# Performance work log

Measured on AMD Instinct MI355X. Metric: run time of the kernel, lower is better.

## Reference

```python
import jax, jax.numpy as jnp
import numpy as np

V, D, H, L, B, S = 32000, 512, 512, 2, 64, 64
PAD = 0
NEG = -1000000000.0


def setup_inputs() -> dict:
    key = jax.random.key(0)
    ks = jax.random.split(key, 12)
    s = 0.05
    X = jax.random.randint(ks[0], (B, S), 0, V)
    enc = jax.random.normal(ks[1], (B, S - 1, H), jnp.float32)
    mask = jnp.zeros((S - 1, S - 1), dtype=bool)
    emb = jax.random.normal(ks[2], (V, D), jnp.float32) * s
    lstm_Wih = jax.random.normal(ks[3], (L, 4 * H, D), jnp.float32) * s  # D == H so stacking works for layer>0
    lstm_Whh = jax.random.normal(ks[4], (L, 4 * H, H), jnp.float32) * s
    lstm_bih = jax.random.normal(ks[5], (L, 4 * H), jnp.float32) * s
    lstm_bhh = jax.random.normal(ks[6], (L, 4 * H), jnp.float32) * s
    attn_Wh = jax.random.normal(ks[7], (H, H), jnp.float32) * s  # attn weight cols acting on decoder hidden
    attn_We = jax.random.normal(ks[8], (H, H), jnp.float32) * s  # attn weight cols acting on encoder outputs
    attn_b = jax.random.normal(ks[9], (H,), jnp.float32) * s
    v_w = jax.random.normal(ks[10], (H,), jnp.float32) * s
    fc_W = jax.random.normal(ks[11], (V, 2 * H), jnp.float32) * s
    fc_b = jnp.zeros((V,), jnp.float32)
    return {"X": X, "encoderOutputs": enc, "mask": mask, "emb": emb,
            "lstm_Wih": lstm_Wih, "lstm_Whh": lstm_Whh, "lstm_bih": lstm_bih, "lstm_bhh": lstm_bhh,
            "attn_Wh": attn_Wh, "attn_We": attn_We, "attn_b": attn_b, "v_w": v_w,
            "fc_W": fc_W, "fc_b": fc_b}


def _forward(X, enc, mask, emb, Wih, Whh, bih, bhh, attn_Wh, attn_We, attn_b, v_w, fc_W, fc_b):
    Bn, Sn = X.shape
    T = Sn - 1
    E = emb[X[:, :-1]]  # [B,T,D]
    # encoder part of attention projection is time-invariant: hoist out of the loop
    enc_proj = jnp.einsum('beh,kh->bek', enc, attn_We) + attn_b  # [B,T,H]
    h0 = jnp.zeros((L, Bn, H), E.dtype)
    c0 = jnp.zeros((L, Bn, H), E.dtype)
    xs = (jnp.transpose(E, (1, 0, 2)), X[:, 1:].T, jnp.arange(T))

    def step(carry, x_t):
        h, c = carry
        e_t, tgt, t = x_t
        inp = e_t
        hs, cs = [], []
        for l in range(L):  # fixed small layer loop
            g = inp @ Wih[l].T + h[l] @ Whh[l].T + bih[l] + bhh[l]
            i, f, gg, o = jnp.split(g, 4, axis=-1)  # torch gate order i,f,g,o
            cn = jax.nn.sigmoid(f) * c[l] + jax.nn.sigmoid(i) * jnp.tanh(gg)
            hn = jax.nn.sigmoid(o) * jnp.tanh(cn)
            hs.append(hn); cs.append(cn)
            inp = hn
        h = jnp.stack(hs); c = jnp.stack(cs)
        top = inp  # [B,H] == LSTM output of last layer
        energy = jnp.tanh((top @ attn_Wh.T)[:, None, :] + enc_proj)  # [B,T,H]
        scores = energy @ v_w  # [B,T]
        # original: self.mask[t-1] (python negative wrap) then mask.unsqueeze(0).unsqueeze(1)
        m = mask[(t - 1) % mask.shape[0], :T]  # [T]
        s3 = jnp.where(m[None, None, :], NEG, scores[None])  # broadcast -> [1,B,T]
        att = jax.nn.softmax(s3, axis=1)[0]  # softmax over batch dim, as in original
        weighted = jnp.einsum('be,beh->bh', att, enc)
        logits = jnp.concatenate([top, weighted], axis=1) @ fc_W.T + fc_b  # [B,V]
        logp = jax.nn.log_softmax(logits, axis=-1)
        nll = -jnp.take_along_axis(logp, tgt[:, None], axis=1)[:, 0]
        valid = tgt != PAD
        loss_t = jnp.sum(jnp.where(valid, nll, 0.0)) / jnp.sum(valid)  # CE mean with ignore_index
        return (h, c), loss_t

    _, losses = jax.lax.scan(step, (h0, c0), xs)
    return jnp.mean(losses)  # totalLoss / (seq_len - 1)


def reference(X, encoderOutputs, mask, emb, lstm_Wih, lstm_Whh, lstm_bih, lstm_bhh, attn_Wh, attn_We, attn_b, v_w, fc_W, fc_b):
    return _forward(X, encoderOutputs, mask, emb, lstm_Wih, lstm_Whh, lstm_bih, lstm_bhh, attn_Wh, attn_We, attn_b, v_w, fc_W, fc_b)
```

## Files before the change

### kernel.cpp

```cpp
#include <hip/hip_runtime.h>
#include <math.h>

#define NEGV -1000000000.0f

typedef unsigned short u16;
typedef __attribute__((ext_vector_type(8))) short bf16x8;
typedef __attribute__((ext_vector_type(4))) float f32x4;

__device__ __forceinline__ u16 f2bf(float f){
  union { float f; unsigned u; } v; v.f = f;
  unsigned u = v.u;
  unsigned r = (u + 0x7fffu + ((u >> 16) & 1u)) >> 16;
  return (u16)r;
}
__device__ __forceinline__ float bf2f(u16 b){
  union { unsigned u; float f; } v; v.u = ((unsigned)b) << 16;
  return v.f;
}
__device__ __forceinline__ float sigmf(float x){ return 1.f / (1.f + __expf(-x)); }
__device__ __forceinline__ float tanhf_(float x){
  float e = __expf(-2.f * fabsf(x));
  float t = (1.f - e) / (1.f + e);
  return x >= 0.f ? t : -t;
}
__device__ __forceinline__ float wred64(float v){
  #pragma unroll
  for (int m = 32; m; m >>= 1) v += __shfl_xor(v, m, 64);
  return v;
}
__device__ __forceinline__ float wmax64(float v){
  #pragma unroll
  for (int m = 32; m; m >>= 1) v = fmaxf(v, __shfl_xor(v, m, 64));
  return v;
}

typedef const __attribute__((address_space(1))) unsigned int* gas_ptr;
typedef __attribute__((address_space(3))) unsigned int* las_ptr;
__device__ __forceinline__ void gl_lds16(const u16* g, u16* l){
  __builtin_amdgcn_global_load_lds((gas_ptr)g, (las_ptr)l, 16, 0, 0);
}

__device__ __forceinline__ void st_sc1_u16(u16* p, unsigned v){
  asm volatile("global_store_short %0, %1, off sc1" :: "v"(p), "v"(v) : "memory");
}

__global__ __launch_bounds__(256) void k_prep(
    const float* wih, const float* whh, const float* we, const float* wh,
    const float* fcw, const float* enc, const float* bih, const float* bhh,
    u16* wihb, u16* whhb, u16* web, u16* whb, u16* fcwb, u16* encb, float* b01)
{
  const long n0 = 2097152, n1 = 2097152, n2 = 262144, n3 = 262144;
  const long n4 = 32768000, n5 = 2064384, n6 = 4096;
  const long total = n0 + n1 + n2 + n3 + n4 + n5 + n6;
  long stride = (long)gridDim.x * 256;
  for (long i = (long)blockIdx.x * 256 + threadIdx.x; i < total; i += stride){
    long j = i;
    if (j < n0){ wihb[j] = f2bf(wih[j]); continue; } j -= n0;
    if (j < n1){ whhb[j] = f2bf(whh[j]); continue; } j -= n1;
    if (j < n2){ web[j]  = f2bf(we[j]);  continue; } j -= n2;
    if (j < n3){ whb[j]  = f2bf(wh[j]);  continue; } j -= n3;
    if (j < n4){ fcwb[j] = f2bf(fcw[j]); continue; } j -= n4;
    if (j < n5){ encb[j] = f2bf(enc[j]); continue; } j -= n5;
    b01[j] = bih[j] + bhh[j];
  }
}

__global__ __launch_bounds__(256) void k_embed(const int* X, const float* emb, u16* ebf){
  int row = blockIdx.x;
  int t = row >> 6, b = row & 63;
  int tok = X[b * 64 + t];
  const float* src = emb + (long)tok * 512;
  u16* dst = ebf + (long)row * 512;
  for (int j = threadIdx.x; j < 512; j += 256) dst[j] = f2bf(src[j]);
}

__global__ __launch_bounds__(256) void gemm_bt(
    const u16* Am, int lda, const u16* Bm, int ldb,
    float* C, int ldc, const float* bias, int K)
{
  __shared__ u16 sA[64 * 32], sB[64 * 32];
  int tm = blockIdx.x, tn = blockIdx.y;
  int tid = threadIdx.x;
  int wave = tid >> 6, lane = tid & 63;
  int wm = wave >> 1, wn = wave & 1;
  int q = lane >> 4, cl = lane & 15;
  f32x4 acc[2][2];
  #pragma unroll
  for (int i = 0; i < 2; i++)
    #pragma unroll
    for (int j = 0; j < 2; j++) acc[i][j] = (f32x4){0.f, 0.f, 0.f, 0.f};

  int r = tid >> 2, ck = tid & 3;
  const u16* Ags = Am + (long)(tm * 64 + r) * lda + ck * 8;
  const u16* Bgs = Bm + (long)(tn * 64 + r) * ldb + ck * 8;
  u16* sAw = &sA[wave * 512];
  u16* sBw = &sB[wave * 512];

  for (int kt = 0; kt < K; kt += 32){
    gl_lds16(Ags + kt, sAw);
    gl_lds16(Bgs + kt, sBw);
    __syncthreads();
    #pragma unroll
    for (int i = 0; i < 2; i++){
      bf16x8 af = *(const bf16x8*)&sA[(wm * 32 + i * 16 + cl) * 32 + q * 8];
      #pragma unroll
      for (int j = 0; j < 2; j++){
        bf16x8 bfv = *(const bf16x8*)&sB[(wn * 32 + j * 16 + cl) * 32 + q * 8];
        acc[i][j] = __builtin_amdgcn_mfma_f32_16x16x32_bf16(af, bfv, acc[i][j], 0, 0, 0);
      }
    }
    __syncthreads();
  }
  #pragma unroll
  for (int i = 0; i < 2; i++)
    #pragma unroll
    for (int j = 0; j < 2; j++){
      int colg = tn * 64 + wn * 32 + j * 16 + cl;
      float bv = bias ? bias[colg] : 0.f;
      #pragma unroll
      for (int rr = 0; rr < 4; rr++){
        int rowg = tm * 64 + wm * 32 + i * 16 + q * 4 + rr;
        C[(long)rowg * ldc + colg] = acc[i][j][rr] + bv;
      }
    }
}

__global__ __launch_bounds__(256) void gemm_btb(
    const u16* Am, int lda, const u16* Bm, int ldb,
    u16* C, int ldc, const float* bias, int K)
{
  __shared__ u16 sA[64 * 32], sB[64 * 32];
  int tm = blockIdx.x, tn = blockIdx.y;
  int tid = threadIdx.x;
  int wave = tid >> 6, lane = tid & 63;
  int wm = wave >> 1, wn = wave & 1;
  int q = lane >> 4, cl = lane & 15;
  f32x4 acc[2][2];
  #pragma unroll
  for (int i = 0; i < 2; i++)
    #pragma unroll
    for (int j = 0; j < 2; j++) acc[i][j] = (f32x4){0.f, 0.f, 0.f, 0.f};

  int r = tid >> 2, ck = tid & 3;
  const u16* Ags = Am + (long)(tm * 64 + r) * lda + ck * 8;
  const u16* Bgs = Bm + (long)(tn * 64 + r) * ldb + ck * 8;
  u16* sAw = &sA[wave * 512];
  u16* sBw = &sB[wave * 512];

  for (int kt = 0; kt < K; kt += 32){
    gl_lds16(Ags + kt, sAw);
    gl_lds16(Bgs + kt, sBw);
    __syncthreads();
    #pragma unroll
    for (int i = 0; i < 2; i++){
      bf16x8 af = *(const bf16x8*)&sA[(wm * 32 + i * 16 + cl) * 32 + q * 8];
      #pragma unroll
      for (int j = 0; j < 2; j++){
        bf16x8 bfv = *(const bf16x8*)&sB[(wn * 32 + j * 16 + cl) * 32 + q * 8];
        acc[i][j] = __builtin_amdgcn_mfma_f32_16x16x32_bf16(af, bfv, acc[i][j], 0, 0, 0);
      }
    }
    __syncthreads();
  }
  #pragma unroll
  for (int i = 0; i < 2; i++)
    #pragma unroll
    for (int j = 0; j < 2; j++){
      int colg = tn * 64 + wn * 32 + j * 16 + cl;
      float bv = bias ? bias[colg] : 0.f;
      #pragma unroll
      for (int rr = 0; rr < 4; rr++){
        int rowg = tm * 64 + wm * 32 + i * 16 + q * 4 + rr;
        C[(long)rowg * ldc + colg] = f2bf(acc[i][j][rr] + bv);
      }
    }
}

__device__ __forceinline__ void wait_flags(int* flags, int tid, int need0, int need1){
  if (tid < 64){
    int need = (tid < 32) ? need0 : need1;
    for (;;){
      int v = __hip_atomic_load(flags + tid, __ATOMIC_RELAXED, __HIP_MEMORY_SCOPE_AGENT);
      if (__ballot(v >= need) == ~0ull) break;
    }
  }
  __syncthreads();
}

#define ISSUE_RING_FRAGS(afr, Ab)                                              \
  {                                                                            \
    _Pragma("unroll")                                                          \
    for (int kt = 0; kt < 16; kt++)                                            \
      asm volatile("global_load_dwordx4 %0, %1, off offset:%2 sc1"             \
                   : "=v"(afr[kt]) : "v"(Ab), "i"(kt * 64));                   \
  }
#define WAITCNT_VM(N)                                                          \
  { asm volatile("s_waitcnt vmcnt(" #N ")" ::: "memory");                      \
    __builtin_amdgcn_sched_barrier(0); }

__global__ __launch_bounds__(256, 1) void lstm_pipe(
    const u16* whh0, const u16* wih1, const u16* whh1,
    const u16* x0b, const float* b1s,
    u16* ring0, u16* ring1, u16* feat, int* flags)
{
  __shared__ u16 sW[32768];
  __shared__ u16 sW2[32768];
  int wg = blockIdx.x;
  int layer = wg >> 5;
  int cc = (wg & 31) * 16;
  int tid = threadIdx.x;
  int wave = tid >> 6, lane = tid & 63;
  int q = lane >> 4, cl = lane & 15;
  int j = cc + cl;

  {
    const u16* src = layer ? whh1 : whh0;
    for (int ch = tid; ch < 4096; ch += 256){
      int row = ch >> 6, c = ch & 63;
      int g = row >> 4, r = row & 15;
      *(uint4*)&sW[((c * 4 + g) * 16 + r) * 8] =
          *(const uint4*)&src[(long)(g * 512 + cc + r) * 512 + c * 8];
      if (layer)
        *(uint4*)&sW2[((c * 4 + g) * 16 + r) * 8] =
            *(const uint4*)&wih1[(long)(g * 512 + cc + r) * 512 + c * 8];
    }
  }
  __syncthreads();

  float cst[4] = {0.f, 0.f, 0.f, 0.f};
  float bg[4];
  if (layer){
    #pragma unroll
    for (int g = 0; g < 4; g++) bg[g] = b1s[g * 512 + j];
  }

  int foff = (wave * 16 + cl) * 512 + q * 8;

  for (int t = 0; t < 63; t++){
    f32x4 acc[4];
    #pragma unroll
    for (int g = 0; g < 4; g++) acc[g] = (f32x4){0.f, 0.f, 0.f, 0.f};

    if (layer == 0){
      float xg[4][4];
      #pragma unroll
      for (int rr = 0; rr < 4; rr++){
        int s = wave * 16 + q * 4 + rr;
        const u16* xr = x0b + (long)(t * 64 + s) * 2048 + j;
        #pragma unroll
        for (int g = 0; g < 4; g++) xg[g][rr] = bf2f(xr[g * 512]);
      }
      wait_flags(flags, tid, t, t - 7);
      {
        const u16* Ab = ring0 + ((t + 7) & 7) * 32768 + foff;
        bf16x8 afr[16];
        ISSUE_RING_FRAGS(afr, Ab);
        WAITCNT_VM(0);
        #pragma unroll
        for (int kt = 0; kt < 16; kt++)
          #pragma unroll
          for (int g = 0; g < 4; g++){
            bf16x8 bfv = *(const bf16x8*)&sW[(((kt * 4 + q) * 4 + g) * 16 + cl) * 8];
            acc[g] = __builtin_amdgcn_mfma_f32_16x16x32_bf16(afr[kt], bfv, acc[g], 0, 0, 0);
          }
      }
      u16* hn = ring0 + (t & 7) * 32768;
      #pragma unroll
      for (int rr = 0; rr < 4; rr++){
        int s = wave * 16 + q * 4 + rr;
        float gi = acc[0][rr] + xg[0][rr];
        float gf = acc[1][rr] + xg[1][rr];
        float gg = acc[2][rr] + xg[2][rr];
        float go = acc[3][rr] + xg[3][rr];
        float cn = sigmf(gf) * cst[rr] + sigmf(gi) * tanhf_(gg);
        cst[rr] = cn;
        st_sc1_u16(hn + s * 512 + j, (unsigned)f2bf(sigmf(go) * tanhf_(cn)));
      }
    } else {
      wait_flags(flags, tid, t + 1, t);
      const u16* Ab1 = ring1 + ((t + 7) & 7) * 32768 + foff;
      const u16* Ab0 = ring0 + (t & 7) * 32768 + foff;
      bf16x8 a1[16], a0[16];
      ISSUE_RING_FRAGS(a1, Ab1);
      ISSUE_RING_FRAGS(a0, Ab0);
      WAITCNT_VM(16);
      #pragma unroll
      for (int kt = 0; kt < 16; kt++)
        #pragma unroll
        for (int g = 0; g < 4; g++){
          bf16x8 bfv = *(const bf16x8*)&sW[(((kt * 4 + q) * 4 + g) * 16 + cl) * 8];
          acc[g] = __builtin_amdgcn_mfma_f32_16x16x32_bf16(a1[kt], bfv, acc[g], 0, 0, 0);
        }
      WAITCNT_VM(0);
      #pragma unroll
      for (int kt = 0; kt < 16; kt++)
        #pragma unroll
        for (int g = 0; g < 4; g++){
          bf16x8 bfv = *(const bf16x8*)&sW2[(((kt * 4 + q) * 4 + g) * 16 + cl) * 8];
          acc[g] = __builtin_amdgcn_mfma_f32_16x16x32_bf16(a0[kt], bfv, acc[g], 0, 0, 0);
        }
      u16* hn = ring1 + (t & 7) * 32768;
      #pragma unroll
      for (int rr = 0; rr < 4; rr++){
        int s = wave * 16 + q * 4 + rr;
        float gi = acc[0][rr] + bg[0];
        float gf = acc[1][rr] + bg[1];
        float gg = acc[2][rr] + bg[2];
        float go = acc[3][rr] + bg[3];
        float cn = sigmf(gf) * cst[rr] + sigmf(gi) * tanhf_(gg);
        cst[rr] = cn;
        u16 hb = f2bf(sigmf(go) * tanhf_(cn));
        st_sc1_u16(hn + s * 512 + j, (unsigned)hb);
        feat[(long)(t * 64 + s) * 1024 + j] = hb;
      }
    }
    asm volatile("s_waitcnt vmcnt(0)" ::: "memory");
    __syncthreads();
    if (tid == 0)
      __hip_atomic_store(flags + wg, t + 1, __ATOMIC_RELAXED, __HIP_MEMORY_SCOPE_AGENT);
  }
}

__global__ __launch_bounds__(256) void k_scores(
    const float* qb, const float* encp, const float* vw, float* scores)
{
  int row = blockIdx.x;
  int b = row & 63;
  int wave = threadIdx.x >> 6, lane = threadIdx.x & 63;
  float qv[8], vwv[8];
  const float* qr = qb + (long)row * 512 + lane * 8;
  #pragma unroll
  for (int i = 0; i < 8; i++){ qv[i] = qr[i]; vwv[i] = vw[lane * 8 + i]; }
  for (int e = wave; e < 63; e += 4){
    const float* er = encp + (long)(b * 63 + e) * 512 + lane * 8;
    float s = 0.f;
    #pragma unroll
    for (int i = 0; i < 8; i++) s += vwv[i] * tanhf_(qv[i] + er[i]);
    s = wred64(s);
    if (lane == 0) scores[(long)row * 63 + e] = s;
  }
}

__global__ __launch_bounds__(64) void k_att(float* scores, const unsigned char* mask){
  int idx = blockIdx.x;
  int t = idx / 63, e = idx - t * 63;
  int lane = threadIdx.x;
  long off = (long)(t * 64 + lane) * 63 + e;
  float s = scores[off];
  if (mask[((t + 62) % 63) * 63 + e]) s = NEGV;
  float M = wmax64(s);
  float p = __expf(s - M);
  float S = wred64(p);
  scores[off] = p / S;
}

__global__ __launch_bounds__(256) void k_weighted(
    const float* att, const float* enc, u16* feat)
{
  int row = blockIdx.x;
  int b = row & 63;
  int j = threadIdx.x;
  float a0 = 0.f, a1 = 0.f;
  const float* ar = att + (long)row * 63;
  const float* er = enc + (long)b * 63 * 512;
  for (int e = 0; e < 63; e++){
    float a = ar[e];
    a0 += a * er[(long)e * 512 + j];
    a1 += a * er[(long)e * 512 + j + 256];
  }
  feat[(long)row * 1024 + 512 + j] = f2bf(a0);
  feat[(long)row * 1024 + 768 + j] = f2bf(a1);
}

__global__ __launch_bounds__(256) void gemm_fc(
    const u16* Am, const u16* Bm, const float* fcb, float* partials)
{
  __shared__ u16 sA[128 * 32], sB[128 * 32];
  __shared__ float sm[128][2], ss[128][2];
  int tm = blockIdx.x, tn = blockIdx.y;
  int tid = threadIdx.x;
  int wave = tid >> 6, lane = tid & 63;
  int wm = wave >> 1, wn = wave & 1;
  int q = lane >> 4, cl = lane & 15;
  f32x4 acc[4][4];
  #pragma unroll
  for (int i = 0; i < 4; i++)
    #pragma unroll
    for (int j = 0; j < 4; j++) acc[i][j] = (f32x4){0.f, 0.f, 0.f, 0.f};

  const u16 *Ag[2], *Bg[2];
  u16 *sAd[2], *sBd[2];
  #pragma unroll
  for (int h = 0; h < 2; h++){
    int idx = h * 256 + tid, rr = idx >> 2, ck = idx & 3;
    Ag[h] = Am + (long)(tm * 128 + rr) * 1024 + ck * 8;
    Bg[h] = Bm + (long)(tn * 128 + rr) * 1024 + ck * 8;
    sAd[h] = &sA[(h * 4 + wave) * 512];
    sBd[h] = &sB[(h * 4 + wave) * 512];
  }
  for (int kt = 0; kt < 1024; kt += 32){
    #pragma unroll
    for (int h = 0; h < 2; h++){
      gl_lds16(Ag[h] + kt, sAd[h]);
      gl_lds16(Bg[h] + kt, sBd[h]);
    }
    __syncthreads();
    bf16x8 afr[4];
    #pragma unroll
    for (int mt = 0; mt < 4; mt++)
      afr[mt] = *(const bf16x8*)&sA[(wm * 64 + mt * 16 + cl) * 32 + q * 8];
    #pragma unroll
    for (int nt = 0; nt < 4; nt++){
      bf16x8 bfv = *(const bf16x8*)&sB[(wn * 64 + nt * 16 + cl) * 32 + q * 8];
      #pragma unroll
      for (int mt = 0; mt < 4; mt++)
        acc[mt][nt] = __builtin_amdgcn_mfma_f32_16x16x32_bf16(afr[mt], bfv, acc[mt][nt], 0, 0, 0);
    }
    __syncthreads();
  }
  float fb[4];
  #pragma unroll
  for (int nt = 0; nt < 4; nt++) fb[nt] = fcb[tn * 128 + wn * 64 + nt * 16 + cl];
  #pragma unroll
  for (int mt = 0; mt < 4; mt++){
    #pragma unroll
    for (int rr = 0; rr < 4; rr++){
      float vals[4];
      float vm = -3.0e38f, vs = 0.f;
      #pragma unroll
      for (int nt = 0; nt < 4; nt++){ float v = acc[mt][nt][rr] + fb[nt]; vals[nt] = v; vm = fmaxf(vm, v); }
      #pragma unroll
      for (int nt = 0; nt < 4; nt++) vs += __expf(vals[nt] - vm);
      #pragma unroll
      for (int m = 1; m < 16; m <<= 1){
        float om = __shfl_xor(vm, m, 16);
        float os = __shfl_xor(vs, m, 16);
        float nm = fmaxf(vm, om);
        vs = vs * __expf(vm - nm) + os * __expf(om - nm);
        vm = nm;
      }
      if (cl == 0){ int rl = wm * 64 + mt * 16 + q * 4 + rr; sm[rl][wn] = vm; ss[rl][wn] = vs; }
    }
  }
  __syncthreads();
  if (tid < 128){
    float m0 = sm[tid][0], m1 = sm[tid][1];
    float M = fmaxf(m0, m1);
    float S = ss[tid][0] * __expf(m0 - M) + ss[tid][1] * __expf(m1 - M);
    long row = tm * 128 + tid;
    partials[(row * 250 + tn) * 2]     = M;
    partials[(row * 250 + tn) * 2 + 1] = S;
  }
}

__global__ __launch_bounds__(256) void k_rowstats(
    const float* partials, const u16* feat, const u16* fcwb,
    const float* fcb, const int* X, float* nll)
{
  int row = blockIdx.x * 4 + (threadIdx.x >> 6);
  int lane = threadIdx.x & 63;
  if (row >= 4032) return;
  float vm = -3.0e38f, vs = 0.f;
  const float* pr = partials + (long)row * 500;
  for (int i = lane; i < 250; i += 64){
    float m = pr[i * 2], s2 = pr[i * 2 + 1];
    float nm = fmaxf(vm, m);
    vs = vs * __expf(vm - nm) + s2 * __expf(m - nm);
    vm = nm;
  }
  #pragma unroll
  for (int m = 32; m; m >>= 1){
    float om = __shfl_xor(vm, m, 64);
    float os = __shfl_xor(vs, m, 64);
    float nm = fmaxf(vm, om);
    vs = vs * __expf(vm - nm) + os * __expf(om - nm);
    vm = nm;
  }
  float logZ = vm + __logf(vs);
  int t = row >> 6, b = row & 63;
  int tgt = X[b * 64 + t + 1];
  const u16* fr = feat + (long)row * 1024 + lane * 16;
  const u16* wr = fcwb + (long)tgt * 1024 + lane * 16;
  float d = 0.f;
  #pragma unroll
  for (int i = 0; i < 16; i++) d += bf2f(fr[i]) * bf2f(wr[i]);
  d = wred64(d);
  if (lane == 0) nll[row] = logZ - (d + fcb[tgt]);
}

__global__ __launch_bounds__(256) void k_final(const float* nll, const int* X, float* out){
  __shared__ float lt[64];
  int wave = threadIdx.x >> 6, lane = threadIdx.x & 63;
  for (int t = wave; t < 63; t += 4){
    int tgt = X[lane * 64 + t + 1];
    float v = (tgt != 0) ? nll[t * 64 + lane] : 0.f;
    float c = (tgt != 0) ? 1.f : 0.f;
    v = wred64(v); c = wred64(c);
    if (lane == 0) lt[t] = v / c;
  }
  __syncthreads();
  if (threadIdx.x == 0){
    float s = 0.f;
    for (int t = 0; t < 63; t++) s += lt[t];
    out[0] = s / 63.f;
  }
}

extern "C" void kernel_launch(void* const* d_in, const int* in_sizes, int n_in,
                              void* d_out, int out_size, void* d_ws, size_t ws_size,
                              hipStream_t stream)
{
  (void)in_sizes; (void)n_in; (void)out_size; (void)ws_size;
  const int*   X    = (const int*)d_in[0];
  const float* enc  = (const float*)d_in[1];
  const unsigned char* mask = (const unsigned char*)d_in[2];
  const float* emb  = (const float*)d_in[3];
  const float* wih  = (const float*)d_in[4];
  const float* whh  = (const float*)d_in[5];
  const float* bih  = (const float*)d_in[6];
  const float* bhh  = (const float*)d_in[7];
  const float* awh  = (const float*)d_in[8];
  const float* awe  = (const float*)d_in[9];
  const float* ab   = (const float*)d_in[10];
  const float* vw   = (const float*)d_in[11];
  const float* fcw  = (const float*)d_in[12];
  const float* fcb  = (const float*)d_in[13];
  float* out = (float*)d_out;

  char* w = (char*)d_ws;
  size_t o = 0;
  auto alloc = [&](size_t bytes){ size_t r = o; o = (o + bytes + 255) & ~(size_t)255; return r; };
  size_t o_ebf  = alloc((size_t)4032 * 512 * 2);
  size_t o_wihb = alloc((size_t)2 * 2048 * 512 * 2);
  size_t o_whhb = alloc((size_t)2 * 2048 * 512 * 2);
  size_t o_web  = alloc((size_t)512 * 512 * 2);
  size_t o_whb  = alloc((size_t)512 * 512 * 2);
  size_t o_fcwb = alloc((size_t)32000 * 1024 * 2);
  size_t o_encb = alloc((size_t)4032 * 512 * 2);
  size_t o_b01  = alloc((size_t)4096 * 4);
  size_t o_x0   = alloc((size_t)4032 * 2048 * 2);
  size_t o_encp = alloc((size_t)4032 * 512 * 4);
  size_t o_q    = alloc((size_t)4032 * 512 * 4);
  size_t o_feat = alloc((size_t)4096 * 1024 * 2);
  size_t o_ring = alloc((size_t)2 * 8 * 32768 * 2);
  size_t o_flags= alloc((size_t)256);
  size_t o_sc   = alloc((size_t)63 * 64 * 63 * 4);
  size_t o_part = alloc((size_t)4096 * 250 * 2 * 4);
  size_t o_nll  = alloc((size_t)4032 * 4);

  u16* ebf   = (u16*)(w + o_ebf);
  u16* wihb  = (u16*)(w + o_wihb);
  u16* whhb  = (u16*)(w + o_whhb);
  u16* web   = (u16*)(w + o_web);
  u16* whb   = (u16*)(w + o_whb);
  u16* fcwb  = (u16*)(w + o_fcwb);
  u16* encb  = (u16*)(w + o_encb);
  float* b01 = (float*)(w + o_b01);
  u16* x0b   = (u16*)(w + o_x0);
  float* encp= (float*)(w + o_encp);
  float* qb  = (float*)(w + o_q);
  u16* feat  = (u16*)(w + o_feat);
  u16* ring0 = (u16*)(w + o_ring);
  u16* ring1 = ring0 + 8 * 32768;
  int* flags = (int*)(w + o_flags);
  float* sc  = (float*)(w + o_sc);
  float* part= (float*)(w + o_part);
  float* nllb= (float*)(w + o_nll);

  hipMemsetAsync(w + o_ring, 0, (o_flags - o_ring) + 256, stream);

  k_prep<<<4096, 256, 0, stream>>>(wih, whh, awe, awh, fcw, enc, bih, bhh,
                                   wihb, whhb, web, whb, fcwb, encb, b01);
  k_embed<<<4032, 256, 0, stream>>>(X, emb, ebf);

  gemm_btb<<<dim3(63, 32), 256, 0, stream>>>(ebf, 512, wihb, 512, x0b, 2048, b01, 512);
  gemm_bt<<<dim3(63, 8), 256, 0, stream>>>(encb, 512, web, 512, encp, 512, ab, 512);

  lstm_pipe<<<64, 256, 0, stream>>>(whhb, wihb + 2048 * 512, whhb + 2048 * 512,
                                    x0b, b01 + 2048, ring0, ring1, feat, flags);

  gemm_bt<<<dim3(63, 8), 256, 0, stream>>>(feat, 1024, whb, 512, qb, 512, nullptr, 512);
  k_scores<<<4032, 256, 0, stream>>>(qb, encp, vw, sc);
  k_att<<<3969, 64, 0, stream>>>(sc, mask);
  k_weighted<<<4032, 256, 0, stream>>>(sc, enc, feat);

  gemm_fc<<<dim3(32, 250), 256, 0, stream>>>(feat, fcwb, fcb, part);
  k_rowstats<<<1008, 256, 0, stream>>>(part, feat, fcwb, fcb, X, nllb);
  k_final<<<1, 256, 0, stream>>>(nllb, X, out);
}
```

Before: 1.298 ms.

## Merge LSTM layers into one wavefront-skewed pipeline on 32 blocks

The persistent LSTM kernel now runs both layers in each of 32 workgroups instead of giving each layer its own 32 workgroups. Layer 1 runs one step behind layer 0, so both share a single global barrier per step. Per-block flag polling is replaced by a per-step atomic counter with sleep-based spinning. Layer 1's input weights are now read from global memory (L2) instead of LDS, since LDS only holds the two recurrent matrices. This halves the number of participating blocks and the barrier traffic, at the cost of more serial MFMA work per block per step and extra global weight reads.

Result: slower. 1.819 ms (+40.1%).

```diff
diff --git a/kernel.cpp b/kernel.cpp
--- a/kernel.cpp
+++ b/kernel.cpp
@@ -176,16 +176,6 @@
     }
 }
 
-__device__ __forceinline__ void wait_flags(int* flags, int tid, int need0, int need1){
-  if (tid < 64){
-    int need = (tid < 32) ? need0 : need1;
-    for (;;){
-      int v = __hip_atomic_load(flags + tid, __ATOMIC_RELAXED, __HIP_MEMORY_SCOPE_AGENT);
-      if (__ballot(v >= need) == ~0ull) break;
-    }
-  }
-  __syncthreads();
-}
 
 #define ISSUE_RING_FRAGS(afr, Ab)                                              \
   {                                                                            \
@@ -201,48 +191,39 @@
 __global__ __launch_bounds__(256, 1) void lstm_pipe(
     const u16* whh0, const u16* wih1, const u16* whh1,
     const u16* x0b, const float* b1s,
-    u16* ring0, u16* ring1, u16* feat, int* flags)
-{
-  __shared__ u16 sW[32768];
-  __shared__ u16 sW2[32768];
+    u16* ring0, u16* ring1, u16* feat, int* done)
+{
+  __shared__ u16 sW0[32768];
+  __shared__ u16 sW1[32768];
   int wg = blockIdx.x;
-  int layer = wg >> 5;
-  int cc = (wg & 31) * 16;
+  int cc = wg * 16;
   int tid = threadIdx.x;
   int wave = tid >> 6, lane = tid & 63;
   int q = lane >> 4, cl = lane & 15;
   int j = cc + cl;
 
-  {
-    const u16* src = layer ? whh1 : whh0;
-    for (int ch = tid; ch < 4096; ch += 256){
-      int row = ch >> 6, c = ch & 63;
-      int g = row >> 4, r = row & 15;
-      *(uint4*)&sW[((c * 4 + g) * 16 + r) * 8] =
-          *(const uint4*)&src[(long)(g * 512 + cc + r) * 512 + c * 8];
-      if (layer)
-        *(uint4*)&sW2[((c * 4 + g) * 16 + r) * 8] =
-            *(const uint4*)&wih1[(long)(g * 512 + cc + r) * 512 + c * 8];
-    }
+  for (int ch = tid; ch < 4096; ch += 256){
+    int row = ch >> 6, c = ch & 63;
+    int g = row >> 4, r = row & 15;
+    *(uint4*)&sW0[((c * 4 + g) * 16 + r) * 8] =
+        *(const uint4*)&whh0[(long)(g * 512 + cc + r) * 512 + c * 8];
+    *(uint4*)&sW1[((c * 4 + g) * 16 + r) * 8] =
+        *(const uint4*)&whh1[(long)(g * 512 + cc + r) * 512 + c * 8];
   }
   __syncthreads();
 
-  float cst[4] = {0.f, 0.f, 0.f, 0.f};
+  float cst0[4] = {0.f, 0.f, 0.f, 0.f};
+  float cst1[4] = {0.f, 0.f, 0.f, 0.f};
   float bg[4];
-  if (layer){
-    #pragma unroll
-    for (int g = 0; g < 4; g++) bg[g] = b1s[g * 512 + j];
-  }
+  #pragma unroll
+  for (int g = 0; g < 4; g++) bg[g] = b1s[g * 512 + j];
 
   int foff = (wave * 16 + cl) * 512 + q * 8;
-
-  for (int t = 0; t < 63; t++){
-    f32x4 acc[4];
-    #pragma unroll
-    for (int g = 0; g < 4; g++) acc[g] = (f32x4){0.f, 0.f, 0.f, 0.f};
-
-    if (layer == 0){
-      float xg[4][4];
+  const u16* wbase = wih1 + (long)(cc + cl) * 512 + q * 8;
+
+  for (int t = 0; t < 64; t++){
+    float xg[4][4];
+    if (t < 63){
       #pragma unroll
       for (int rr = 0; rr < 4; rr++){
         int s = wave * 16 + q * 4 + rr;
@@ -250,74 +231,90 @@
         #pragma unroll
         for (int g = 0; g < 4; g++) xg[g][rr] = bf2f(xr[g * 512]);
       }
-      wait_flags(flags, tid, t, t - 7);
-      {
-        const u16* Ab = ring0 + ((t + 7) & 7) * 32768 + foff;
-        bf16x8 afr[16];
-        ISSUE_RING_FRAGS(afr, Ab);
-        WAITCNT_VM(0);
-        #pragma unroll
-        for (int kt = 0; kt < 16; kt++)
-          #pragma unroll
-          for (int g = 0; g < 4; g++){
-            bf16x8 bfv = *(const bf16x8*)&sW[(((kt * 4 + q) * 4 + g) * 16 + cl) * 8];
-            acc[g] = __builtin_amdgcn_mfma_f32_16x16x32_bf16(afr[kt], bfv, acc[g], 0, 0, 0);
-          }
-      }
-      u16* hn = ring0 + (t & 7) * 32768;
-      #pragma unroll
-      for (int rr = 0; rr < 4; rr++){
-        int s = wave * 16 + q * 4 + rr;
-        float gi = acc[0][rr] + xg[0][rr];
-        float gf = acc[1][rr] + xg[1][rr];
-        float gg = acc[2][rr] + xg[2][rr];
-        float go = acc[3][rr] + xg[3][rr];
-        float cn = sigmf(gf) * cst[rr] + sigmf(gi) * tanhf_(gg);
-        cst[rr] = cn;
-        st_sc1_u16(hn + s * 512 + j, (unsigned)f2bf(sigmf(go) * tanhf_(cn)));
-      }
-    } else {
-      wait_flags(flags, tid, t + 1, t);
-      const u16* Ab1 = ring1 + ((t + 7) & 7) * 32768 + foff;
-      const u16* Ab0 = ring0 + (t & 7) * 32768 + foff;
-      bf16x8 a1[16], a0[16];
-      ISSUE_RING_FRAGS(a1, Ab1);
-      ISSUE_RING_FRAGS(a0, Ab0);
-      WAITCNT_VM(16);
+    }
+    if (t > 0){
+      if (tid < 64){
+        const int* dp = done + (t - 1);
+        for (;;){
+          int v = __hip_atomic_load(dp, __ATOMIC_RELAXED, __HIP_MEMORY_SCOPE_AGENT);
+          if (__ballot(v >= 32)) break;
+          __builtin_amdgcn_s_sleep(1);
+        }
+      }
+      __syncthreads();
+    }
+
+    bf16x8 a0[16], a1[16];
+    const u16* Ab0 = ring0 + ((t + 7) & 7) * 32768 + foff;
+    const u16* Ab1 = ring1 + ((t + 6) & 7) * 32768 + foff;
+    ISSUE_RING_FRAGS(a0, Ab0);
+    ISSUE_RING_FRAGS(a1, Ab1);
+    WAITCNT_VM(16);
+
+    if (t < 63){
+      f32x4 acc0[4];
+      #pragma unroll
+      for (int g = 0; g < 4; g++) acc0[g] = (f32x4){0.f, 0.f, 0.f, 0.f};
       #pragma unroll
       for (int kt = 0; kt < 16; kt++)
         #pragma unroll
         for (int g = 0; g < 4; g++){
-          bf16x8 bfv = *(const bf16x8*)&sW[(((kt * 4 + q) * 4 + g) * 16 + cl) * 8];
-          acc[g] = __builtin_amdgcn_mfma_f32_16x16x32_bf16(a1[kt], bfv, acc[g], 0, 0, 0);
+          bf16x8 bfv = *(const bf16x8*)&sW0[(((kt * 4 + q) * 4 + g) * 16 + cl) * 8];
+          acc0[g] = __builtin_amdgcn_mfma_f32_16x16x32_bf16(a0[kt], bfv, acc0[g], 0, 0, 0);
         }
-      WAITCNT_VM(0);
+      u16* hn = ring0 + (t & 7) * 32768;
+      #pragma unroll
+      for (int rr = 0; rr < 4; rr++){
+        int s = wave * 16 + q * 4 + rr;
+        float gi = acc0[0][rr] + xg[0][rr];
+        float gf = acc0[1][rr] + xg[1][rr];
+        float gg = acc0[2][rr] + xg[2][rr];
+        float go = acc0[3][rr] + xg[3][rr];
+        float cn = sigmf(gf) * cst0[rr] + sigmf(gi) * tanhf_(gg);
+        cst0[rr] = cn;
+        st_sc1_u16(hn + s * 512 + j, (unsigned)f2bf(sigmf(go) * tanhf_(cn)));
+      }
+    }
+
+    if (t > 0){
+      f32x4 acc1[4];
+      #pragma unroll
+      for (int g = 0; g < 4; g++) acc1[g] = (f32x4){0.f, 0.f, 0.f, 0.f};
       #pragma unroll
       for (int kt = 0; kt < 16; kt++)
         #pragma unroll
         for (int g = 0; g < 4; g++){
-          bf16x8 bfv = *(const bf16x8*)&sW2[(((kt * 4 + q) * 4 + g) * 16 + cl) * 8];
-          acc[g] = __builtin_amdgcn_mfma_f32_16x16x32_bf16(a0[kt], bfv, acc[g], 0, 0, 0);
+          bf16x8 bfv = *(const bf16x8*)(wbase + (long)g * 262144 + kt * 32);
+          acc1[g] = __builtin_amdgcn_mfma_f32_16x16x32_bf16(a0[kt], bfv, acc1[g], 0, 0, 0);
         }
-      u16* hn = ring1 + (t & 7) * 32768;
+      WAITCNT_VM(0);
+      #pragma unroll
+      for (int kt = 0; kt < 16; kt++)
+        #pragma unroll
+        for (int g = 0; g < 4; g++){
+          bf16x8 bfv = *(const bf16x8*)&sW1[(((kt * 4 + q) * 4 + g) * 16 + cl) * 8];
+          acc1[g] = __builtin_amdgcn_mfma_f32_16x16x32_bf16(a1[kt], bfv, acc1[g], 0, 0, 0);
+        }
+      u16* hn = ring1 + ((t + 7) & 7) * 32768;
       #pragma unroll
       for (int rr = 0; rr < 4; rr++){
         int s = wave * 16 + q * 4 + rr;
-        float gi = acc[0][rr] + bg[0];
-        float gf = acc[1][rr] + bg[1];
-        float gg = acc[2][rr] + bg[2];
-        float go = acc[3][rr] + bg[3];
-        float cn = sigmf(gf) * cst[rr] + sigmf(gi) * tanhf_(gg);
-        cst[rr] = cn;
+        float gi = acc1[0][rr] + bg[0];
+        float gf = acc1[1][rr] + bg[1];
+        float gg = acc1[2][rr] + bg[2];
+        float go = acc1[3][rr] + bg[3];
+        float cn = sigmf(gf) * cst1[rr] + sigmf(gi) * tanhf_(gg);
+        cst1[rr] = cn;
         u16 hb = f2bf(sigmf(go) * tanhf_(cn));
         st_sc1_u16(hn + s * 512 + j, (unsigned)hb);
-        feat[(long)(t * 64 + s) * 1024 + j] = hb;
-      }
-    }
+        feat[(long)((t - 1) * 64 + s) * 1024 + j] = hb;
+      }
+    }
+
     asm volatile("s_waitcnt vmcnt(0)" ::: "memory");
     __syncthreads();
     if (tid == 0)
-      __hip_atomic_store(flags + wg, t + 1, __ATOMIC_RELAXED, __HIP_MEMORY_SCOPE_AGENT);
+      (void)__hip_atomic_fetch_add(done + t, 1, __ATOMIC_RELAXED, __HIP_MEMORY_SCOPE_AGENT);
   }
 }
 
@@ -543,7 +540,7 @@
   size_t o_q    = alloc((size_t)4032 * 512 * 4);
   size_t o_feat = alloc((size_t)4096 * 1024 * 2);
   size_t o_ring = alloc((size_t)2 * 8 * 32768 * 2);
-  size_t o_flags= alloc((size_t)256);
+  size_t o_done = alloc((size_t)256);
   size_t o_sc   = alloc((size_t)63 * 64 * 63 * 4);
   size_t o_part = alloc((size_t)4096 * 250 * 2 * 4);
   size_t o_nll  = alloc((size_t)4032 * 4);
@@ -562,12 +559,12 @@
   u16* feat  = (u16*)(w + o_feat);
   u16* ring0 = (u16*)(w + o_ring);
   u16* ring1 = ring0 + 8 * 32768;
-  int* flags = (int*)(w + o_flags);
+  int* done  = (int*)(w + o_done);
   float* sc  = (float*)(w + o_sc);
   float* part= (float*)(w + o_part);
   float* nllb= (float*)(w + o_nll);
 
-  hipMemsetAsync(w + o_ring, 0, (o_flags - o_ring) + 256, stream);
+  hipMemsetAsync(w + o_ring, 0, (o_done - o_ring) + 256, stream);
 
   k_prep<<<4096, 256, 0, stream>>>(wih, whh, awe, awh, fcw, enc, bih, bhh,
                                    wihb, whhb, web, whb, fcwb, encb, b01);
@@ -576,8 +573,8 @@
   gemm_btb<<<dim3(63, 32), 256, 0, stream>>>(ebf, 512, wihb, 512, x0b, 2048, b01, 512);
   gemm_bt<<<dim3(63, 8), 256, 0, stream>>>(encb, 512, web, 512, encp, 512, ab, 512);
 
-  lstm_pipe<<<64, 256, 0, stream>>>(whhb, wihb + 2048 * 512, whhb + 2048 * 512,
-                                    x0b, b01 + 2048, ring0, ring1, feat, flags);
+  lstm_pipe<<<32, 256, 0, stream>>>(whhb, wihb + 2048 * 512, whhb + 2048 * 512,
+                                    x0b, b01 + 2048, ring0, ring1, feat, done);
 
   gemm_bt<<<dim3(63, 8), 256, 0, stream>>>(feat, 1024, whb, 512, qb, 512, nullptr, 512);
   k_scores<<<4032, 256, 0, stream>>>(qb, encp, vw, sc);
```

## Use per-step counters for LSTM pipeline sync and double-buffer FC GEMM tiles

Applied to the files above, without the earlier changes.

Each LSTM pipeline step now waits on a single per-timestep atomic counter that the 32 workgroups of a layer increment, replacing 64 per-workgroup flag reads in the spin loop. This reduces polling traffic on the cross-workgroup barrier that sits on the recurrent critical path. Separately, the big FC GEMM gets double-buffered LDS tiles, so the next K slice is prefetched while MFMAs run on the current one. This doubles LDS use in that kernel, which may limit occupancy.

Measured after the change: 1.329 ms. 1.02x slower.

```diff
diff --git a/kernel.cpp b/kernel.cpp
--- a/kernel.cpp
+++ b/kernel.cpp
@@ -176,12 +176,13 @@
     }
 }
 
-__device__ __forceinline__ void wait_flags(int* flags, int tid, int need0, int need1){
+__device__ __forceinline__ void wait_cnt2(const int* p0, const int* p1, int tid){
   if (tid < 64){
-    int need = (tid < 32) ? need0 : need1;
+    const int* p = (tid < 32) ? p0 : p1;
     for (;;){
-      int v = __hip_atomic_load(flags + tid, __ATOMIC_RELAXED, __HIP_MEMORY_SCOPE_AGENT);
-      if (__ballot(v >= need) == ~0ull) break;
+      int v = p ? __hip_atomic_load(p, __ATOMIC_RELAXED, __HIP_MEMORY_SCOPE_AGENT)
+                : 32;
+      if (__ballot(v >= 32) == ~0ull) break;
     }
   }
   __syncthreads();
@@ -201,10 +202,12 @@
 __global__ __launch_bounds__(256, 1) void lstm_pipe(
     const u16* whh0, const u16* wih1, const u16* whh1,
     const u16* x0b, const float* b1s,
-    u16* ring0, u16* ring1, u16* feat, int* flags)
+    u16* ring0, u16* ring1, u16* feat, int* done)
 {
   __shared__ u16 sW[32768];
   __shared__ u16 sW2[32768];
+  int* done0 = done;
+  int* done1 = done + 64;
   int wg = blockIdx.x;
   int layer = wg >> 5;
   int cc = (wg & 31) * 16;
@@ -250,7 +253,8 @@
         #pragma unroll
         for (int g = 0; g < 4; g++) xg[g][rr] = bf2f(xr[g * 512]);
       }
-      wait_flags(flags, tid, t, t - 7);
+      wait_cnt2(t > 0 ? done0 + (t - 1) : nullptr,
+                t >= 8 ? done1 + (t - 8) : nullptr, tid);
       {
         const u16* Ab = ring0 + ((t + 7) & 7) * 32768 + foff;
         bf16x8 afr[16];
@@ -277,7 +281,7 @@
         st_sc1_u16(hn + s * 512 + j, (unsigned)f2bf(sigmf(go) * tanhf_(cn)));
       }
     } else {
-      wait_flags(flags, tid, t + 1, t);
+      wait_cnt2(done0 + t, t > 0 ? done1 + (t - 1) : nullptr, tid);
       const u16* Ab1 = ring1 + ((t + 7) & 7) * 32768 + foff;
       const u16* Ab0 = ring0 + (t & 7) * 32768 + foff;
       bf16x8 a1[16], a0[16];
@@ -317,7 +321,8 @@
     asm volatile("s_waitcnt vmcnt(0)" ::: "memory");
     __syncthreads();
     if (tid == 0)
-      __hip_atomic_store(flags + wg, t + 1, __ATOMIC_RELAXED, __HIP_MEMORY_SCOPE_AGENT);
+      (void)__hip_atomic_fetch_add((layer ? done1 : done0) + t, 1,
+                                   __ATOMIC_RELAXED, __HIP_MEMORY_SCOPE_AGENT);
   }
 }
 
@@ -375,7 +380,7 @@
 __global__ __launch_bounds__(256) void gemm_fc(
     const u16* Am, const u16* Bm, const float* fcb, float* partials)
 {
-  __shared__ u16 sA[128 * 32], sB[128 * 32];
+  __shared__ u16 sA[2][128 * 32], sB[2][128 * 32];
   __shared__ float sm[128][2], ss[128][2];
   int tm = blockIdx.x, tn = blockIdx.y;
   int tid = threadIdx.x;
@@ -389,34 +394,42 @@
     for (int j = 0; j < 4; j++) acc[i][j] = (f32x4){0.f, 0.f, 0.f, 0.f};
 
   const u16 *Ag[2], *Bg[2];
-  u16 *sAd[2], *sBd[2];
+  int sOff[2];
   #pragma unroll
   for (int h = 0; h < 2; h++){
     int idx = h * 256 + tid, rr = idx >> 2, ck = idx & 3;
     Ag[h] = Am + (long)(tm * 128 + rr) * 1024 + ck * 8;
     Bg[h] = Bm + (long)(tn * 128 + rr) * 1024 + ck * 8;
-    sAd[h] = &sA[(h * 4 + wave) * 512];
-    sBd[h] = &sB[(h * 4 + wave) * 512];
-  }
+    sOff[h] = (h * 4 + wave) * 512;
+  }
+  #pragma unroll
+  for (int h = 0; h < 2; h++){
+    gl_lds16(Ag[h], &sA[0][sOff[h]]);
+    gl_lds16(Bg[h], &sB[0][sOff[h]]);
+  }
+  __syncthreads();
+  int cur = 0;
   for (int kt = 0; kt < 1024; kt += 32){
-    #pragma unroll
-    for (int h = 0; h < 2; h++){
-      gl_lds16(Ag[h] + kt, sAd[h]);
-      gl_lds16(Bg[h] + kt, sBd[h]);
-    }
-    __syncthreads();
+    if (kt + 32 < 1024){
+      #pragma unroll
+      for (int h = 0; h < 2; h++){
+        gl_lds16(Ag[h] + kt + 32, &sA[cur ^ 1][sOff[h]]);
+        gl_lds16(Bg[h] + kt + 32, &sB[cur ^ 1][sOff[h]]);
+      }
+    }
     bf16x8 afr[4];
     #pragma unroll
     for (int mt = 0; mt < 4; mt++)
-      afr[mt] = *(const bf16x8*)&sA[(wm * 64 + mt * 16 + cl) * 32 + q * 8];
+      afr[mt] = *(const bf16x8*)&sA[cur][(wm * 64 + mt * 16 + cl) * 32 + q * 8];
     #pragma unroll
     for (int nt = 0; nt < 4; nt++){
-      bf16x8 bfv = *(const bf16x8*)&sB[(wn * 64 + nt * 16 + cl) * 32 + q * 8];
+      bf16x8 bfv = *(const bf16x8*)&sB[cur][(wn * 64 + nt * 16 + cl) * 32 + q * 8];
       #pragma unroll
       for (int mt = 0; mt < 4; mt++)
         acc[mt][nt] = __builtin_amdgcn_mfma_f32_16x16x32_bf16(afr[mt], bfv, acc[mt][nt], 0, 0, 0);
     }
     __syncthreads();
+    cur ^= 1;
   }
   float fb[4];
   #pragma unroll
@@ -543,7 +556,7 @@
   size_t o_q    = alloc((size_t)4032 * 512 * 4);
   size_t o_feat = alloc((size_t)4096 * 1024 * 2);
   size_t o_ring = alloc((size_t)2 * 8 * 32768 * 2);
-  size_t o_flags= alloc((size_t)256);
+  size_t o_done = alloc((size_t)512);
   size_t o_sc   = alloc((size_t)63 * 64 * 63 * 4);
   size_t o_part = alloc((size_t)4096 * 250 * 2 * 4);
   size_t o_nll  = alloc((size_t)4032 * 4);
@@ -562,12 +575,12 @@
   u16* feat  = (u16*)(w + o_feat);
   u16* ring0 = (u16*)(w + o_ring);
   u16* ring1 = ring0 + 8 * 32768;
-  int* flags = (int*)(w + o_flags);
+  int* done  = (int*)(w + o_done);
   float* sc  = (float*)(w + o_sc);
   float* part= (float*)(w + o_part);
   float* nllb= (float*)(w + o_nll);
 
-  hipMemsetAsync(w + o_ring, 0, (o_flags - o_ring) + 256, stream);
+  hipMemsetAsync(w + o_ring, 0, (o_done - o_ring) + 512, stream);
 
   k_prep<<<4096, 256, 0, stream>>>(wih, whh, awe, awh, fcw, enc, bih, bhh,
                                    wihb, whhb, web, whb, fcwb, encb, b01);
@@ -577,7 +590,7 @@
   gemm_bt<<<dim3(63, 8), 256, 0, stream>>>(encb, 512, web, 512, encp, 512, ab, 512);
 
   lstm_pipe<<<64, 256, 0, stream>>>(whhb, wihb + 2048 * 512, whhb + 2048 * 512,
-                                    x0b, b01 + 2048, ring0, ring1, feat, flags);
+                                    x0b, b01 + 2048, ring0, ring1, feat, done);
 
   gemm_bt<<<dim3(63, 8), 256, 0, stream>>>(feat, 1024, whb, 512, qb, 512, nullptr, 512);
   k_scores<<<4032, 256, 0, stream>>>(qb, encp, vw, sc);
```

## Enlarge FC GEMM tiles with double-buffered swizzled LDS and vectorize weight conversion

Applied to the files above, without the earlier changes.

The vocabulary projection GEMM moves from 128x128 tiles with 256 threads to 256x256 tiles with 512 threads. It uses 64-wide K chunks with XOR-swizzled LDS layout and double-buffered global-to-LDS prefetch that overlaps with the MFMAs, and raises wave priority around the MFMA block. The partial softmax stats are reduced across 4 N-waves, which halves the partials per row, and the row-stats kernel is adjusted to match. The prep conversion kernel now processes four floats per thread with vector loads and stores. The larger tile improves operand reuse and bandwidth, at the cost of high register pressure and a single block per CU.

New measurement: 1.270 ms. -2.2%, faster.

```diff
diff --git a/kernel.cpp b/kernel.cpp
--- a/kernel.cpp
+++ b/kernel.cpp
@@ -44,6 +44,12 @@
   asm volatile("global_store_short %0, %1, off sc1" :: "v"(p), "v"(v) : "memory");
 }
 
+__device__ __forceinline__ void cvt4(u16* d, const float* s){
+  float4 v = *(const float4*)s;
+  union { u16 h[4]; uint2 u; } o;
+  o.h[0] = f2bf(v.x); o.h[1] = f2bf(v.y); o.h[2] = f2bf(v.z); o.h[3] = f2bf(v.w);
+  *(uint2*)d = o.u;
+}
 __global__ __launch_bounds__(256) void k_prep(
     const float* wih, const float* whh, const float* we, const float* wh,
     const float* fcw, const float* enc, const float* bih, const float* bhh,
@@ -51,17 +57,19 @@
 {
   const long n0 = 2097152, n1 = 2097152, n2 = 262144, n3 = 262144;
   const long n4 = 32768000, n5 = 2064384, n6 = 4096;
-  const long total = n0 + n1 + n2 + n3 + n4 + n5 + n6;
+  const long total4 = (n0 + n1 + n2 + n3 + n4 + n5 + n6) >> 2;
   long stride = (long)gridDim.x * 256;
-  for (long i = (long)blockIdx.x * 256 + threadIdx.x; i < total; i += stride){
-    long j = i;
-    if (j < n0){ wihb[j] = f2bf(wih[j]); continue; } j -= n0;
-    if (j < n1){ whhb[j] = f2bf(whh[j]); continue; } j -= n1;
-    if (j < n2){ web[j]  = f2bf(we[j]);  continue; } j -= n2;
-    if (j < n3){ whb[j]  = f2bf(wh[j]);  continue; } j -= n3;
-    if (j < n4){ fcwb[j] = f2bf(fcw[j]); continue; } j -= n4;
-    if (j < n5){ encb[j] = f2bf(enc[j]); continue; } j -= n5;
-    b01[j] = bih[j] + bhh[j];
+  for (long i = (long)blockIdx.x * 256 + threadIdx.x; i < total4; i += stride){
+    long j = i << 2;
+    if (j < n0){ cvt4(wihb + j, wih + j); continue; } j -= n0;
+    if (j < n1){ cvt4(whhb + j, whh + j); continue; } j -= n1;
+    if (j < n2){ cvt4(web + j,  we + j);  continue; } j -= n2;
+    if (j < n3){ cvt4(whb + j,  wh + j);  continue; } j -= n3;
+    if (j < n4){ cvt4(fcwb + j, fcw + j); continue; } j -= n4;
+    if (j < n5){ cvt4(encb + j, enc + j); continue; } j -= n5;
+    float4 a = *(const float4*)(bih + j);
+    float4 b = *(const float4*)(bhh + j);
+    *(float4*)(b01 + j) = make_float4(a.x + b.x, a.y + b.y, a.z + b.z, a.w + b.w);
   }
 }
 
@@ -372,57 +380,84 @@
   feat[(long)row * 1024 + 768 + j] = f2bf(a1);
 }
 
-__global__ __launch_bounds__(256) void gemm_fc(
+__global__ __launch_bounds__(512, 1) void gemm_fc(
     const u16* Am, const u16* Bm, const float* fcb, float* partials)
 {
-  __shared__ u16 sA[128 * 32], sB[128 * 32];
-  __shared__ float sm[128][2], ss[128][2];
+  __shared__ u16 sA[2][16384], sB[2][16384];
+  __shared__ float sm[256][4], ss[256][4];
   int tm = blockIdx.x, tn = blockIdx.y;
   int tid = threadIdx.x;
   int wave = tid >> 6, lane = tid & 63;
-  int wm = wave >> 1, wn = wave & 1;
+  int wm = wave >> 2, wn = wave & 3;
   int q = lane >> 4, cl = lane & 15;
-  f32x4 acc[4][4];
-  #pragma unroll
-  for (int i = 0; i < 4; i++)
+
+  f32x4 acc[8][4];
+  #pragma unroll
+  for (int i = 0; i < 8; i++)
     #pragma unroll
     for (int j = 0; j < 4; j++) acc[i][j] = (f32x4){0.f, 0.f, 0.f, 0.f};
 
-  const u16 *Ag[2], *Bg[2];
-  u16 *sAd[2], *sBd[2];
-  #pragma unroll
-  for (int h = 0; h < 2; h++){
-    int idx = h * 256 + tid, rr = idx >> 2, ck = idx & 3;
-    Ag[h] = Am + (long)(tm * 128 + rr) * 1024 + ck * 8;
-    Bg[h] = Bm + (long)(tn * 128 + rr) * 1024 + ck * 8;
-    sAd[h] = &sA[(h * 4 + wave) * 512];
-    sBd[h] = &sB[(h * 4 + wave) * 512];
-  }
-  for (int kt = 0; kt < 1024; kt += 32){
-    #pragma unroll
-    for (int h = 0; h < 2; h++){
-      gl_lds16(Ag[h] + kt, sAd[h]);
-      gl_lds16(Bg[h] + kt, sBd[h]);
-    }
+  const u16 *pA[4], *pB[4];
+  int sdst[4];
+  #pragma unroll
+  for (int h = 0; h < 4; h++){
+    int c = tid + h * 512;
+    int row = c >> 3;
+    int kc = (c & 7) ^ (row & 7);
+    pA[h] = Am + (long)(tm * 256 + row) * 1024 + kc * 8;
+    pB[h] = Bm + (long)(tn * 256 + row) * 1024 + kc * 8;
+    sdst[h] = (h * 512 + wave * 64) * 8;
+  }
+  int r0 = cl * 64;
+  int ex = (cl & 7) * 16;
+  int e0 = ((q * 16) ^ ex) >> 1;
+  int e1 = ((64 + q * 16) ^ ex) >> 1;
+
+  #pragma unroll
+  for (int h = 0; h < 4; h++){
+    gl_lds16(pA[h], &sA[0][sdst[h]]);
+    gl_lds16(pB[h], &sB[0][sdst[h]]);
+  }
+  asm volatile("s_waitcnt vmcnt(0)" ::: "memory");
+  __syncthreads();
+
+  for (int k = 0; k < 16; k++){
+    int cur = k & 1;
+    if (k < 15){
+      int adv = (k + 1) * 64;
+      #pragma unroll
+      for (int h = 0; h < 4; h++){
+        gl_lds16(pA[h] + adv, &sA[cur ^ 1][sdst[h]]);
+        gl_lds16(pB[h] + adv, &sB[cur ^ 1][sdst[h]]);
+      }
+    }
+    #pragma unroll
+    for (int ks = 0; ks < 2; ks++){
+      int eo = ks ? e1 : e0;
+      bf16x8 af[8], bf[4];
+      #pragma unroll
+      for (int mt = 0; mt < 8; mt++)
+        af[mt] = *(const bf16x8*)&sA[cur][(wm * 8 + mt) * 1024 + r0 + eo];
+      #pragma unroll
+      for (int nt = 0; nt < 4; nt++)
+        bf[nt] = *(const bf16x8*)&sB[cur][(wn * 4 + nt) * 1024 + r0 + eo];
+      __builtin_amdgcn_s_setprio(1);
+      #pragma unroll
+      for (int nt = 0; nt < 4; nt++)
+        #pragma unroll
+        for (int mt = 0; mt < 8; mt++)
+          acc[mt][nt] = __builtin_amdgcn_mfma_f32_16x16x32_bf16(af[mt], bf[nt], acc[mt][nt], 0, 0, 0);
+      __builtin_amdgcn_s_setprio(0);
+    }
+    asm volatile("s_waitcnt vmcnt(0)" ::: "memory");
     __syncthreads();
-    bf16x8 afr[4];
-    #pragma unroll
-    for (int mt = 0; mt < 4; mt++)
-      afr[mt] = *(const bf16x8*)&sA[(wm * 64 + mt * 16 + cl) * 32 + q * 8];
-    #pragma unroll
-    for (int nt = 0; nt < 4; nt++){
-      bf16x8 bfv = *(const bf16x8*)&sB[(wn * 64 + nt * 16 + cl) * 32 + q * 8];
-      #pragma unroll
-      for (int mt = 0; mt < 4; mt++)
-        acc[mt][nt] = __builtin_amdgcn_mfma_f32_16x16x32_bf16(afr[mt], bfv, acc[mt][nt], 0, 0, 0);
-    }
-    __syncthreads();
-  }
+  }
+
   float fb[4];
   #pragma unroll
-  for (int nt = 0; nt < 4; nt++) fb[nt] = fcb[tn * 128 + wn * 64 + nt * 16 + cl];
-  #pragma unroll
-  for (int mt = 0; mt < 4; mt++){
+  for (int nt = 0; nt < 4; nt++) fb[nt] = fcb[tn * 256 + wn * 64 + nt * 16 + cl];
+  #pragma unroll
+  for (int mt = 0; mt < 8; mt++){
     #pragma unroll
     for (int rr = 0; rr < 4; rr++){
       float vals[4];
@@ -439,17 +474,23 @@
         vs = vs * __expf(vm - nm) + os * __expf(om - nm);
         vm = nm;
       }
-      if (cl == 0){ int rl = wm * 64 + mt * 16 + q * 4 + rr; sm[rl][wn] = vm; ss[rl][wn] = vs; }
+      if (cl == 0){
+        int rl = wm * 128 + mt * 16 + q * 4 + rr;
+        sm[rl][wn] = vm; ss[rl][wn] = vs;
+      }
     }
   }
   __syncthreads();
-  if (tid < 128){
-    float m0 = sm[tid][0], m1 = sm[tid][1];
-    float M = fmaxf(m0, m1);
-    float S = ss[tid][0] * __expf(m0 - M) + ss[tid][1] * __expf(m1 - M);
-    long row = tm * 128 + tid;
-    partials[(row * 250 + tn) * 2]     = M;
-    partials[(row * 250 + tn) * 2 + 1] = S;
+  if (tid < 256){
+    float M = -3.0e38f;
+    #pragma unroll
+    for (int w = 0; w < 4; w++) M = fmaxf(M, sm[tid][w]);
+    float S = 0.f;
+    #pragma unroll
+    for (int w = 0; w < 4; w++) S += ss[tid][w] * __expf(sm[tid][w] - M);
+    long row = tm * 256 + tid;
+    partials[(row * 125 + tn) * 2]     = M;
+    partials[(row * 125 + tn) * 2 + 1] = S;
   }
 }
 
@@ -461,8 +502,8 @@
   int lane = threadIdx.x & 63;
   if (row >= 4032) return;
   float vm = -3.0e38f, vs = 0.f;
-  const float* pr = partials + (long)row * 500;
-  for (int i = lane; i < 250; i += 64){
+  const float* pr = partials + (long)row * 250;
+  for (int i = lane; i < 125; i += 64){
     float m = pr[i * 2], s2 = pr[i * 2 + 1];
     float nm = fmaxf(vm, m);
     vs = vs * __expf(vm - nm) + s2 * __expf(m - nm);
@@ -543,7 +584,7 @@
   size_t o_q    = alloc((size_t)4032 * 512 * 4);
   size_t o_feat = alloc((size_t)4096 * 1024 * 2);
   size_t o_ring = alloc((size_t)2 * 8 * 32768 * 2);
-  size_t o_flags= alloc((size_t)256);
+  size_t o_flags= alloc((size_t)512);
   size_t o_sc   = alloc((size_t)63 * 64 * 63 * 4);
   size_t o_part = alloc((size_t)4096 * 250 * 2 * 4);
   size_t o_nll  = alloc((size_t)4032 * 4);
@@ -567,7 +608,7 @@
   float* part= (float*)(w + o_part);
   float* nllb= (float*)(w + o_nll);
 
-  hipMemsetAsync(w + o_ring, 0, (o_flags - o_ring) + 256, stream);
+  hipMemsetAsync(w + o_ring, 0, (o_flags - o_ring) + 512, stream);
 
   k_prep<<<4096, 256, 0, stream>>>(wih, whh, awe, awh, fcw, enc, bih, bhh,
                                    wihb, whhb, web, whb, fcwb, encb, b01);
@@ -584,7 +625,7 @@
   k_att<<<3969, 64, 0, stream>>>(sc, mask);
   k_weighted<<<4032, 256, 0, stream>>>(sc, enc, feat);
 
-  gemm_fc<<<dim3(32, 250), 256, 0, stream>>>(feat, fcwb, fcb, part);
+  gemm_fc<<<dim3(16, 125), 512, 0, stream>>>(feat, fcwb, fcb, part);
   k_rowstats<<<1008, 256, 0, stream>>>(part, feat, fcwb, fcb, X, nllb);
   k_final<<<1, 256, 0, stream>>>(nllb, X, out);
 }
```
